# Performance work log

Measured on AMD Instinct MI355X. Metric: run time of the kernel, lower is better.

The kernel has to match this reference:

```python
import jax, jax.numpy as jnp
import numpy as np


def setup_inputs() -> dict:
    key = jax.random.key(0)
    k1, k2, k3 = jax.random.split(key, 3)
    N, M, D = 8192, 8192, 128
    feat = jax.random.normal(k1, (N, D), dtype=jnp.float32)
    feat2 = jax.random.normal(k2, (M, D), dtype=jnp.float32)
    labels = jax.random.randint(k3, (N,), 0, M, dtype=jnp.int64)
    temp = jnp.array(1.0, dtype=jnp.float32)
    return {"feat": feat, "feat2": feat2, "temp": temp, "labels": labels}


def reference(feat, feat2, temp, labels):
    # (same math as sqrt(sum((x[:,None]-y)**2, -1)) but without the N*M*D intermediate).
    x_sq = jnp.sum(feat * feat, axis=-1)    # [N]
    y_sq = jnp.sum(feat2 * feat2, axis=-1)  # [M]
    sq_dist = x_sq[:, None] + y_sq[None, :] - 2.0 * (feat @ feat2.T)  # [N, M]
    dist = jnp.sqrt(jnp.maximum(sq_dist, 0.0))
    logits = -temp * dist                    # [N, M]
    # Cross-entropy with mean reduction (nn.CrossEntropyLoss default)
    log_z = jax.nn.logsumexp(logits, axis=-1)                              # [N]
    picked = jnp.take_along_axis(logits, labels[:, None], axis=1)[:, 0]   # [N]
    return jnp.mean(log_z - picked)
```

## Files before the change

kernel.cpp:

```cpp
#include <hip/hip_runtime.h>
#include <hip/hip_bf16.h>
#include <stdint.h>

#define NR 8192
#define MC 8192
#define DD 128
#define MSPLIT 16
#define CPB 512
#define TILES 16
#define ROWBLK 64
#define GRID ((NR / ROWBLK) * MSPLIT)

typedef __attribute__((ext_vector_type(8))) short short8;
typedef __attribute__((ext_vector_type(16))) float f32x16;

__device__ __forceinline__ ushort bf16r(float f) {
    __hip_bfloat16 h = __float2bfloat16(f);
    return *(ushort*)&h;
}

__device__ __forceinline__ void gload_lds16(const void* g, void* l) {
    __builtin_amdgcn_global_load_lds(
        (const __attribute__((address_space(1))) uint32_t*)g,
        (__attribute__((address_space(3))) uint32_t*)l, 16, 0, 0);
}
__device__ __forceinline__ void gload_lds4(const void* g, void* l) {
    __builtin_amdgcn_global_load_lds(
        (const __attribute__((address_space(1))) uint32_t*)g,
        (__attribute__((address_space(3))) uint32_t*)l, 4, 0, 0);
}

__global__ __launch_bounds__(256) void prep_kernel(
    const float* __restrict__ feat, const float* __restrict__ feat2,
    const float* __restrict__ temp_p, const int* __restrict__ labels,
    ushort* __restrict__ fb, ushort* __restrict__ f2bf,
    float* __restrict__ xsq2, float* __restrict__ ysq2,
    float* __restrict__ pick, float* __restrict__ consts) {
    int b = blockIdx.x;
    if (b < 2048) {
        int row = b * 4 + (threadIdx.x >> 6);
        int l = threadIdx.x & 63;
        float temp = *temp_p;
        float c = temp * 1.4426950408889634f;
        float c2 = c * c;
        int lab = labels[row];
        float2 x = ((const float2*)(feat  + (size_t)row * DD))[l];
        float2 y = ((const float2*)(feat2 + (size_t)row * DD))[l];
        float2 z = ((const float2*)(feat2 + (size_t)lab * DD))[l];
        ushort2 ux; ux.x = bf16r(x.x); ux.y = bf16r(x.y);
        ((ushort2*)(fb + (size_t)row * DD))[l] = ux;
        float sx = x.x * x.x + x.y * x.y;
        float sy = y.x * y.x + y.y * y.y;
        float d0 = x.x - z.x, d1 = x.y - z.y;
        float sd = d0 * d0 + d1 * d1;
        #pragma unroll
        for (int off = 1; off < 64; off <<= 1) {
            sx += __shfl_xor(sx, off);
            sy += __shfl_xor(sy, off);
            sd += __shfl_xor(sd, off);
        }
        if (l == 0) {
            xsq2[row] = c2 * sx;
            ysq2[row] = c2 * sy;
            pick[row] = temp * __builtin_amdgcn_sqrtf(sd);
            if (row == 0) consts[0] = -2.0f * c2;
        }
    } else {
        int id = (b - 2048) * 256 + threadIdx.x;
        int slot = id & 63;
        int ks = (id >> 6) & 7;
        int tile = id >> 9;
        int col = tile * 32 + (slot & 31);
        int k0 = ks * 16 + (slot >> 5) * 8;
        const float* src = feat2 + (size_t)col * DD + k0;
        float4 v0 = ((const float4*)src)[0];
        float4 v1 = ((const float4*)src)[1];
        short8 o;
        o[0] = (short)bf16r(v0.x); o[1] = (short)bf16r(v0.y);
        o[2] = (short)bf16r(v0.z); o[3] = (short)bf16r(v0.w);
        o[4] = (short)bf16r(v1.x); o[5] = (short)bf16r(v1.y);
        o[6] = (short)bf16r(v1.z); o[7] = (short)bf16r(v1.w);
        ((short8*)f2bf)[id] = o;
    }
}

__global__ __launch_bounds__(128, 4) void main_kernel(
    const ushort* __restrict__ fb, const ushort* __restrict__ f2bf,
    const float* __restrict__ xsq2, const float* __restrict__ ysq2,
    const float* __restrict__ consts, float* __restrict__ spart) {
    __shared__ ushort lds[2][8 * 512];
    __shared__ float ys_lds[CPB];

    int bid = blockIdx.x;
    int cs = bid & (MSPLIT - 1);
    int rb = bid >> 4;
    int tid = threadIdx.x;
    int wave = tid >> 6, lane = tid & 63;
    int lcol = lane & 31, lhalf = lane >> 5;
    int rowbase = rb * ROWBLK + wave * 32;
    int tile0 = cs * TILES;
    float m2c2 = consts[0];

    short8 a[8];
    const ushort* ap = fb + (size_t)(rowbase + lcol) * DD + lhalf * 8;
    #pragma unroll
    for (int ks = 0; ks < 8; ++ks) a[ks] = *(const short8*)(ap + ks * 16);

    float xs2[16];
    #pragma unroll
    for (int r = 0; r < 16; ++r)
        xs2[r] = xsq2[rowbase + (r & 3) + 8 * (r >> 2) + 4 * lhalf];

    float s[16];
    #pragma unroll
    for (int r = 0; r < 16; ++r) s[r] = 0.f;

    {
        const float* ysrc = ysq2 + cs * CPB;
        #pragma unroll
        for (int c = 0; c < 4; ++c) {
            int ch = wave * 4 + c;
            gload_lds4(ysrc + ch * 64 + lane, &ys_lds[ch * 64]);
        }
        #pragma unroll
        for (int c = 0; c < 4; ++c) {
            int ch = wave * 4 + c;
            gload_lds16(f2bf + ((size_t)tile0 * 8 + ch) * 512 + lane * 8,
                        &lds[0][ch * 512]);
        }
    }

    #pragma unroll 1
    for (int t = 0; t < TILES; ++t) {
        asm volatile("s_waitcnt vmcnt(0)" ::: "memory");
        __builtin_amdgcn_s_barrier();
        if (t + 1 < TILES) {
            #pragma unroll
            for (int c = 0; c < 4; ++c) {
                int ch = wave * 4 + c;
                gload_lds16(f2bf + ((size_t)(tile0 + t + 1) * 8 + ch) * 512 + lane * 8,
                            &lds[(t + 1) & 1][ch * 512]);
            }
        }

        float ysv = ys_lds[t * 32 + lcol];
        const ushort* lb = &lds[t & 1][0];
        f32x16 acc;
        #pragma unroll
        for (int r = 0; r < 16; ++r) acc[r] = 0.f;
        __builtin_amdgcn_s_setprio(1);
        #pragma unroll
        for (int ks = 0; ks < 8; ++ks) {
            short8 bf = *(const short8*)(lb + ks * 512 + lane * 8);
            acc = __builtin_amdgcn_mfma_f32_32x32x16_bf16(a[ks], bf, acc, 0, 0, 0);
        }
        __builtin_amdgcn_s_setprio(0);
        #pragma unroll
        for (int r = 0; r < 16; ++r) {
            float q = fmaf(m2c2, acc[r], xs2[r] + ysv);
            s[r] += __builtin_amdgcn_exp2f(-__builtin_amdgcn_sqrtf(__builtin_fabsf(q)));
        }
    }

    #pragma unroll
    for (int off = 1; off <= 16; off <<= 1)
        #pragma unroll
        for (int r = 0; r < 16; ++r) s[r] += __shfl_xor(s[r], off);

    if (lcol == 0) {
        float* sp = spart + (size_t)cs * NR + rowbase;
        #pragma unroll
        for (int r = 0; r < 16; ++r)
            sp[(r & 3) + 8 * (r >> 2) + 4 * lhalf] = s[r];
    }
}

__global__ __launch_bounds__(256) void finish1_kernel(
    const float* __restrict__ spart, const float* __restrict__ pick,
    float* __restrict__ partial) {
    __shared__ float red[4];
    int row = blockIdx.x * 256 + threadIdx.x;
    float ssum = 0.f;
    #pragma unroll
    for (int ms = 0; ms < MSPLIT; ++ms) ssum += spart[(size_t)ms * NR + row];
    float v = __builtin_amdgcn_logf(ssum) * 0.6931471805599453f + pick[row];
    #pragma unroll
    for (int off = 1; off < 64; off <<= 1) v += __shfl_xor(v, off);
    if ((threadIdx.x & 63) == 0) red[threadIdx.x >> 6] = v;
    __syncthreads();
    if (threadIdx.x == 0) partial[blockIdx.x] = red[0] + red[1] + red[2] + red[3];
}

__global__ void finish2_kernel(const float* __restrict__ partial, float* __restrict__ out) {
    float v = (threadIdx.x < 32) ? partial[threadIdx.x] : 0.f;
    #pragma unroll
    for (int off = 1; off < 64; off <<= 1) v += __shfl_xor(v, off);
    if (threadIdx.x == 0) out[0] = v * (1.0f / NR);
}

extern "C" void kernel_launch(void* const* d_in, const int* in_sizes, int n_in,
                              void* d_out, int out_size, void* d_ws, size_t ws_size,
                              hipStream_t stream) {
    const float* feat   = (const float*)d_in[0];
    const float* feat2  = (const float*)d_in[1];
    const float* temp   = (const float*)d_in[2];
    const int*   labels = (const int*)d_in[3];
    float* out = (float*)d_out;

    char* ws = (char*)d_ws;
    ushort* fb    = (ushort*)ws;
    ushort* f2bf  = (ushort*)(ws + (2u << 20));
    float*  xsq2  = (float*)(ws + (4u << 20));
    float*  ysq2  = xsq2 + NR;
    float*  pick  = ysq2 + MC;
    float*  consts  = pick + NR;
    float*  partial = consts + 16;
    float*  spart = (float*)(ws + (5u << 20));

    prep_kernel<<<2560, 256, 0, stream>>>(feat, feat2, temp, labels,
                                          fb, f2bf, xsq2, ysq2, pick, consts);
    main_kernel<<<GRID, 128, 0, stream>>>(fb, f2bf, xsq2, ysq2, consts, spart);
    finish1_kernel<<<NR / 256, 256, 0, stream>>>(spart, pick, partial);
    finish2_kernel<<<1, 64, 0, stream>>>(partial, out);
}
```

Baseline: 45.03 us.

## Software-pipeline MFMA tiles with double accumulators to overlap epilogue

Restructures the main loop so each tile's MFMA chain is issued into one accumulator while the previous tile's exp/sqrt epilogue runs from the other. The goal is to hide the transcendental epilogue latency behind matrix-core work instead of serializing them. It adds 16 more accumulator registers per lane, which could reduce occupancy under the 128x4 launch bounds, and the loop is manually unrolled by two with a prologue and tail.

```diff
diff --git a/kernel.cpp b/kernel.cpp
--- a/kernel.cpp
+++ b/kernel.cpp
@@ -130,37 +130,77 @@
         }
     }
 
+    f32x16 accA, accB;
+    float ysA = 0.f, ysB = 0.f;
+
+    #define STAGE_NEXT(T)                                                          \
+        if ((T) + 1 < TILES) {                                                     \
+            _Pragma("unroll")                                                      \
+            for (int c = 0; c < 4; ++c) {                                          \
+                int ch = wave * 4 + c;                                             \
+                gload_lds16(f2bf + ((size_t)(tile0 + (T) + 1) * 8 + ch) * 512      \
+                                 + lane * 8, &lds[((T) + 1) & 1][ch * 512]);       \
+            }                                                                      \
+        }
+    #define MFMA_TILE(T, ACC)                                                      \
+        {                                                                          \
+            const ushort* lb = &lds[(T) & 1][0];                                   \
+            _Pragma("unroll")                                                      \
+            for (int r = 0; r < 16; ++r) (ACC)[r] = 0.f;                           \
+            __builtin_amdgcn_s_setprio(1);                                         \
+            _Pragma("unroll")                                                      \
+            for (int ks = 0; ks < 8; ++ks) {                                       \
+                short8 bf = *(const short8*)(lb + ks * 512 + lane * 8);            \
+                (ACC) = __builtin_amdgcn_mfma_f32_32x32x16_bf16(a[ks], bf, (ACC),  \
+                                                                0, 0, 0);          \
+            }                                                                      \
+            __builtin_amdgcn_s_setprio(0);                                         \
+        }
+    #define EPILOGUE(PACC, PYS)                                                    \
+        {                                                                          \
+            _Pragma("unroll")                                                      \
+            for (int r = 0; r < 16; ++r) {                                         \
+                float q = fmaf(m2c2, (PACC)[r], xs2[r] + (PYS));                   \
+                s[r] += __builtin_amdgcn_exp2f(                                    \
+                            -__builtin_amdgcn_sqrtf(__builtin_fabsf(q)));          \
+            }                                                                      \
+        }
+
+    asm volatile("s_waitcnt vmcnt(0)" ::: "memory");
+    __builtin_amdgcn_s_barrier();
+    STAGE_NEXT(0)
+    ysA = ys_lds[0 * 32 + lcol];
+    MFMA_TILE(0, accA)
+
     #pragma unroll 1
-    for (int t = 0; t < TILES; ++t) {
+    for (int j = 0; j < (TILES - 2) / 2; ++j) {
+        int t1 = 2 * j + 1;
         asm volatile("s_waitcnt vmcnt(0)" ::: "memory");
         __builtin_amdgcn_s_barrier();
-        if (t + 1 < TILES) {
-            #pragma unroll
-            for (int c = 0; c < 4; ++c) {
-                int ch = wave * 4 + c;
-                gload_lds16(f2bf + ((size_t)(tile0 + t + 1) * 8 + ch) * 512 + lane * 8,
-                            &lds[(t + 1) & 1][ch * 512]);
-            }
-        }
-
-        float ysv = ys_lds[t * 32 + lcol];
-        const ushort* lb = &lds[t & 1][0];
-        f32x16 acc;
-        #pragma unroll
-        for (int r = 0; r < 16; ++r) acc[r] = 0.f;
-        __builtin_amdgcn_s_setprio(1);
-        #pragma unroll
-        for (int ks = 0; ks < 8; ++ks) {
-            short8 bf = *(const short8*)(lb + ks * 512 + lane * 8);
-            acc = __builtin_amdgcn_mfma_f32_32x32x16_bf16(a[ks], bf, acc, 0, 0, 0);
-        }
-        __builtin_amdgcn_s_setprio(0);
-        #pragma unroll
-        for (int r = 0; r < 16; ++r) {
-            float q = fmaf(m2c2, acc[r], xs2[r] + ysv);
-            s[r] += __builtin_amdgcn_exp2f(-__builtin_amdgcn_sqrtf(__builtin_fabsf(q)));
-        }
-    }
+        STAGE_NEXT(t1)
+        ysB = ys_lds[t1 * 32 + lcol];
+        MFMA_TILE(t1, accB)
+        EPILOGUE(accA, ysA)
+
+        int t2 = 2 * j + 2;
+        asm volatile("s_waitcnt vmcnt(0)" ::: "memory");
+        __builtin_amdgcn_s_barrier();
+        STAGE_NEXT(t2)
+        ysA = ys_lds[t2 * 32 + lcol];
+        MFMA_TILE(t2, accA)
+        EPILOGUE(accB, ysB)
+    }
+
+    asm volatile("s_waitcnt vmcnt(0)" ::: "memory");
+    __builtin_amdgcn_s_barrier();
+    ysB = ys_lds[15 * 32 + lcol];
+    MFMA_TILE(15, accB)
+    EPILOGUE(accA, ysA)
+    EPILOGUE(accB, ysB)
+
+    #undef STAGE_NEXT
+    #undef MFMA_TILE
+    #undef EPILOGUE
 
     #pragma unroll
     for (int off = 1; off <= 16; off <<= 1)
```

After: 81.83 us. 1.82x slower.
